# Kernel tuning notes

Hardware: AMD Instinct MI355X
Metric: run time of the kernel (lower is better)

Reference implementation:

```python
import jax, jax.numpy as jnp
import numpy as np


def _normalize(x):
    # channel mean-subtract then channel L2 normalize, as in MIDMs.forward
    x = x - x.mean(axis=1, keepdims=True)
    return x / jnp.linalg.norm(x, axis=1, keepdims=True)


def setup_inputs() -> dict:
    key = jax.random.key(0)
    ks = jax.random.split(key, 6)
    B, C, H, W = 2, 256, 64, 64
    return {
        "trg_out": jax.random.normal(ks[0], (B, C, H, W), jnp.float32),
        "src_out": jax.random.normal(ks[1], (B, C, H, W), jnp.float32),
        "ref_out": jax.random.normal(ks[2], (B, C, H, W), jnp.float32),
        "src_feats": jax.random.normal(ks[3], (B, 4, H, W), jnp.float32),
        "ref_feats": jax.random.normal(ks[4], (B, 4, H, W), jnp.float32),
        "ref_semantics": jax.random.uniform(ks[5], (B, 151, H, W), jnp.float32),
    }


def reference(trg_out, src_out, ref_out, src_feats, ref_feats, ref_semantics):
    B, C, H, W = trg_out.shape
    L = H * W
    # normalized matching features, flattened over spatial positions
    t = _normalize(trg_out).reshape(B, C, L)   # [B, C, Lt]
    s = _normalize(src_out).reshape(B, C, L)   # [B, C, Ls]
    r = _normalize(ref_out).reshape(B, C, L)

    # Correlation.correlation: dense cosine affinity between all position pairs
    corr_src = jnp.einsum("bci,bcj->bij", t, s)  # [B, Lt, Ls]
    corr_ref = jnp.einsum("bci,bcj->bij", t, r)

    # soft_warp: softmax over source positions, attention-weighted gather
    attn_src = jax.nn.softmax(corr_src, axis=-1)
    attn_ref = jax.nn.softmax(corr_ref, axis=-1)

    warped_src_feat = jnp.einsum("bij,bcj->bci", attn_src,
                                 src_feats.reshape(B, -1, L)).reshape(B, -1, H, W)
    warped_ref_feat = jnp.einsum("bij,bcj->bci", attn_ref,
                                 ref_feats.reshape(B, -1, L)).reshape(B, -1, H, W)
    warped_ref_seg = jnp.einsum("bij,bcj->bci", attn_ref,
                                ref_semantics.reshape(B, -1, L)).reshape(B, -1, H, W)
    return warped_src_feat, warped_ref_feat, warped_ref_seg
```

## Files before the change

### kernel.cpp

```cpp
#include <hip/hip_runtime.h>
#include <hip/hip_bf16.h>
#include <cstdint>
#include <cstddef>

typedef unsigned short u16;
typedef __attribute__((ext_vector_type(8))) __bf16 bf16x8;
typedef __attribute__((ext_vector_type(4))) unsigned u32x4;
typedef __attribute__((ext_vector_type(16))) float f32x16;

#define LPOS 4096
#define CDIM 256
#define LDSBUF 13312

#if __has_builtin(__builtin_amdgcn_exp2f)
#define EXP2(x) __builtin_amdgcn_exp2f(x)
#else
#define EXP2(x) exp2f(x)
#endif

#define GLOAD_LDS16(g, l)                                                      \
  __builtin_amdgcn_global_load_lds(                                            \
      (const __attribute__((address_space(1))) void*)(g),                      \
      (__attribute__((address_space(3))) void*)(l), 16, 0, 0)

__device__ __forceinline__ unsigned f2bfbits(float x) {
  union { float f; unsigned u; } v; v.f = x;
  return (v.u + 0x7FFFu + ((v.u >> 16) & 1u)) >> 16;
}
__device__ __forceinline__ unsigned packbf(float a, float b) {
  __hip_bfloat162 h2 = __float22bfloat162_rn(make_float2(a, b));
  return *(unsigned*)&h2;
}

__global__ void norm_fused(const float* __restrict__ t_in,
                           const float* __restrict__ s_in,
                           const float* __restrict__ r_in,
                           u16* __restrict__ qn, u16* __restrict__ ksn,
                           u16* __restrict__ krn) {
  __shared__ float tile[256 * 33];
  __shared__ float sums[256], sqs[256];
  __shared__ float mv[32], ivv[32];
  int idx = blockIdx.x;
  int ab = idx >> 7, lt = idx & 127;
  int arr = ab >> 1, b = ab & 1;
  int l0 = lt * 32;
  const float* inp = (arr == 0 ? t_in : arr == 1 ? s_in : r_in) + (size_t)b * CDIM * LPOS;
  u16* outp = (arr == 0 ? qn : arr == 1 ? ksn : krn) + (size_t)b * LPOS * CDIM;
  float scale = (arr == 0) ? 1.4426950408889634f : 1.0f;
  int t = threadIdx.x;
  int cg = t >> 5, l = t & 31;
  float sum = 0.f, sq = 0.f;
#pragma unroll 8
  for (int cc = 0; cc < 32; ++cc) {
    int c = cg * 32 + cc;
    float v = inp[(size_t)c * LPOS + l0 + l];
    tile[c * 33 + l] = v;
    sum += v; sq += v * v;
  }
  sums[t] = sum; sqs[t] = sq;
  __syncthreads();
  if (t < 32) {
    float s = 0.f, q = 0.f;
#pragma unroll
    for (int g = 0; g < 8; ++g) { s += sums[g * 32 + t]; q += sqs[g * 32 + t]; }
    float mean = s * (1.0f / CDIM);
    float nsq = q - s * s * (1.0f / CDIM);
    mv[t] = mean;
    ivv[t] = rsqrtf(fmaxf(nsq, 1e-20f)) * scale;
  }
  __syncthreads();
  int c2 = t & 127, ph = t >> 7;
#pragma unroll 4
  for (int rr = 0; rr < 16; ++rr) {
    int pos = ph + rr * 2;
    float m = mv[pos], iv = ivv[pos];
    float v0 = (tile[(2 * c2) * 33 + pos] - m) * iv;
    float v1 = (tile[(2 * c2 + 1) * 33 + pos] - m) * iv;
    *(unsigned*)&outp[(size_t)(l0 + pos) * CDIM + 2 * c2] = packbf(v0, v1);
  }
}

__global__ void build_v(const float* __restrict__ sf, const float* __restrict__ rf,
                        const float* __restrict__ sem,
                        u16* __restrict__ vs, u16* __restrict__ vr) {
  int t = blockIdx.x * 256 + threadIdx.x;
  const int NVS = 2 * 32 * 4096;
  if (t < NVS) {
    int b = t >> 17;
    int c = (t >> 12) & 31;
    int j = t & 4095;
    float v = (c < 4) ? sf[((size_t)b * 4 + c) * LPOS + j] : (c == 4 ? 1.0f : 0.0f);
    vs[t] = (u16)f2bfbits(v);
  } else {
    int t2 = t - NVS;
    if (t2 < 2 * 160 * 4096) {
      int b = t2 / (160 * 4096);
      int rr = t2 % (160 * 4096);
      int c = rr >> 12, j = rr & 4095;
      float v = (c < 151) ? sem[((size_t)b * 151 + c) * LPOS + j]
              : (c < 155) ? rf[((size_t)b * 4 + (c - 151)) * LPOS + j]
              : (c == 155) ? 1.0f : 0.0f;
      vr[((size_t)b * 160 + c) * LPOS + j] = (u16)f2bfbits(v);
    }
  }
}

template <int CT>
__device__ __forceinline__ void flash_body(
    const u16* __restrict__ qb, const u16* __restrict__ kb,
    const u16* __restrict__ vb, float* __restrict__ dst,
    u16 (*lds)[LDSBUF], int wave, int lane, int i_wave, int j_base, int iters) {
  int h = lane >> 5, ln = lane & 31;

  bf16x8 qf[16];
  const u16* qrow = qb + (size_t)(i_wave + ln) * CDIM;
#pragma unroll
  for (int kt = 0; kt < 16; ++kt)
    qf[kt] = *(const bf16x8*)(qrow + kt * 16 + h * 8);
#pragma unroll
  for (int kt = 0; kt < 16; ++kt)
    asm volatile("" : "+v"(*(u32x4*)&qf[kt]));

  f32x16 O[CT];
#pragma unroll
  for (int c = 0; c < CT; ++c)
#pragma unroll
    for (int t = 0; t < 16; ++t) O[c][t] = 0.0f;

  auto stage = [&](int j0s, int buf) {
#pragma unroll
    for (int g = 0; g < 4; ++g) {
      int G = wave * 4 + g;
      int j = 2 * G + h;
      GLOAD_LDS16(kb + (size_t)(j0s + j) * CDIM + (ln ^ (j & 7)) * 8,
                  &lds[buf][G * 512]);
    }
    if constexpr (CT == 5) {
#pragma unroll
      for (int g = 0; g < 3; ++g) {
        int s = wave + g * 4;
        if (s < 10) {
          int f = s * 64 + lane;
          int p = f / 160;
          int c = f - p * 160;
          GLOAD_LDS16(vb + (size_t)c * LPOS + j0s + p * 8,
                      &lds[buf][8192 + s * 512]);
        }
      }
    }
  };

  int kread_base = ln * 256 + 8 * (h ^ (ln & 1));
  int q = (ln >> 1) & 3;
  const u16* ka[4];
#pragma unroll
  for (int m = 0; m < 4; ++m) ka[m] = &lds[0][kread_base + 16 * (m ^ q)];
  const u16* va = &lds[0][8192 + h * 1280 + ln * 8];

  f32x16 Sp;
#pragma unroll
  for (int t = 0; t < 16; ++t) Sp[t] = 0.0f;

  auto finish_prev = [&](int pbo, const bf16x8* vfp) {
    f32x16 S;
#pragma unroll
    for (int t = 0; t < 16; ++t) S[t] = EXP2(Sp[t]);
    bf16x8 pb[2];
#pragma unroll
    for (int kh = 0; kh < 2; ++kh) {
      unsigned c0 = packbf(S[kh * 8 + 0], S[kh * 8 + 1]);
      unsigned c1 = packbf(S[kh * 8 + 2], S[kh * 8 + 3]);
      unsigned c2 = packbf(S[kh * 8 + 4], S[kh * 8 + 5]);
      unsigned c3 = packbf(S[kh * 8 + 6], S[kh * 8 + 7]);
      asm("v_permlane32_swap_b32 %0, %1" : "+v"(c0), "+v"(c2));
      asm("v_permlane32_swap_b32 %0, %1" : "+v"(c1), "+v"(c3));
      union { unsigned u[4]; bf16x8 v; } tmp;
      tmp.u[0] = c0;
      tmp.u[1] = c1;
      tmp.u[2] = c2;
      tmp.u[3] = c3;
      pb[kh] = tmp.v;
    }
#pragma unroll
    for (int ct = 0; ct < CT; ++ct)
#pragma unroll
      for (int kt2 = 0; kt2 < 2; ++kt2) {
        bf16x8 vax;
        if constexpr (CT == 5)
          vax = *(const bf16x8*)(va + kt2 * 2560 + ct * 256 + pbo);
        else
          vax = vfp[kt2];
        O[ct] = __builtin_amdgcn_mfma_f32_32x32x16_bf16(vax, pb[kt2], O[ct], 0, 0, 0);
      }
  };

  stage(j_base, 0);

  int buf = 0, pbo = 0;
  for (int jt = 0; jt < iters; ++jt) {
    int j0 = j_base + jt * 32;
    int bo = buf * LDSBUF;

    asm volatile("s_waitcnt vmcnt(0)" ::: "memory");
    __builtin_amdgcn_sched_barrier(0);
    __builtin_amdgcn_s_barrier();
    __builtin_amdgcn_sched_barrier(0);

    bf16x8 vf[2];
    if (CT == 1 && jt >= 1) {
#pragma unroll
      for (int kt2 = 0; kt2 < 2; ++kt2)
        vf[kt2] = *(const bf16x8*)(vb + (size_t)ln * LPOS + (j0 - 32) + (2 * kt2 + h) * 8);
    }
    if (jt + 1 < iters) {
      int nb = (buf == 2) ? 0 : buf + 1;
      stage(j0 + 32, nb);
    }

    __builtin_amdgcn_s_setprio(1);

    f32x16 Sa, Sb;
#pragma unroll
    for (int t = 0; t < 16; ++t) { Sa[t] = 0.0f; Sb[t] = 0.0f; }
#pragma unroll
    for (int kt = 0; kt < 16; kt += 2) {
      bf16x8 ka0 = *(const bf16x8*)(ka[kt & 3] + 64 * (kt >> 2) + bo);
      Sa = __builtin_amdgcn_mfma_f32_32x32x16_bf16(ka0, qf[kt], Sa, 0, 0, 0);
      bf16x8 ka1 = *(const bf16x8*)(ka[(kt + 1) & 3] + 64 * ((kt + 1) >> 2) + bo);
      Sb = __builtin_amdgcn_mfma_f32_32x32x16_bf16(ka1, qf[kt + 1], Sb, 0, 0, 0);
    }

    if (jt >= 1) finish_prev(pbo, vf);

#pragma unroll
    for (int t = 0; t < 16; ++t) Sp[t] = Sa[t] + Sb[t];

    __builtin_amdgcn_s_setprio(0);

    pbo = bo;
    buf = (buf == 2) ? 0 : buf + 1;
  }

  {
    bf16x8 vf[2];
    if constexpr (CT == 1) {
      int jlast = j_base + (iters - 1) * 32;
#pragma unroll
      for (int kt2 = 0; kt2 < 2; ++kt2)
        vf[kt2] = *(const bf16x8*)(vb + (size_t)ln * LPOS + jlast + (2 * kt2 + h) * 8);
    }
    finish_prev(pbo, vf);
  }

  const int climit = (CT == 1) ? 5 : 156;
#pragma unroll
  for (int ct = 0; ct < CT; ++ct)
#pragma unroll
    for (int t = 0; t < 16; ++t) {
      int c = ct * 32 + (t & 3) + 8 * (t >> 2) + 4 * h;
      if (c < climit)
        dst[(size_t)c * LPOS + i_wave + ln] = O[ct][t];
    }
}

__global__ __launch_bounds__(256, 2) void flash(
    const u16* __restrict__ qn, const u16* __restrict__ ksn, const u16* __restrict__ krn,
    const u16* __restrict__ vs, const u16* __restrict__ vr,
    float* __restrict__ nsrc, float* __restrict__ nref,
    int nch_src, int nch_ref) {
  __shared__ u16 lds[3][LDSBUF];
  int tid = threadIdx.x;
  int wave = tid >> 6, lane = tid & 63;
  int idx = blockIdx.x;
  int nrefb = 64 * nch_ref;
  if (idx < nrefb) {
    int r = idx;
    int chunk = r >> 6, b = (r >> 5) & 1, wgi = r & 31;
    int jchunk = LPOS / nch_ref;
    flash_body<5>(qn + (size_t)b * LPOS * CDIM, krn + (size_t)b * LPOS * CDIM,
                  vr + (size_t)b * 160 * LPOS,
                  nref + (size_t)(chunk * 2 + b) * 160 * LPOS,
                  lds, wave, lane, wgi * 128 + wave * 32, chunk * jchunk,
                  jchunk / 32);
  } else {
    int r = idx - nrefb;
    int chunk = r >> 6, b = (r >> 5) & 1, wgi = r & 31;
    int jchunk = LPOS / nch_src;
    flash_body<1>(qn + (size_t)b * LPOS * CDIM, ksn + (size_t)b * LPOS * CDIM,
                  vs + (size_t)b * 32 * LPOS,
                  nsrc + (size_t)(chunk * 2 + b) * 32 * LPOS,
                  lds, wave, lane, wgi * 128 + wave * 32, chunk * jchunk,
                  jchunk / 32);
  }
}

__global__ void finalize(const float* __restrict__ nsrc, const float* __restrict__ nref,
                         float* __restrict__ out, int nch_src, int nch_ref) {
  int v = blockIdx.x * 256 + threadIdx.x;
  if (v >= 325632) return;
  float nx = 0.f, ny = 0.f, nz = 0.f, nw = 0.f;
  float dx = 0.f, dy = 0.f, dz = 0.f, dw = 0.f;
  if (v < 8192) {
    int b = v >> 12, c = (v >> 10) & 3, i4 = v & 1023;
    for (int k = 0; k < nch_src; ++k) {
      const float* base = nsrc + ((size_t)(k * 2 + b) * 32) * LPOS;
      float4 n4 = ((const float4*)(base + (size_t)c * LPOS))[i4];
      float4 d4 = ((const float4*)(base + (size_t)4 * LPOS))[i4];
      nx += n4.x; ny += n4.y; nz += n4.z; nw += n4.w;
      dx += d4.x; dy += d4.y; dz += d4.z; dw += d4.w;
    }
  } else if (v < 16384) {
    int v1 = v - 8192;
    int b = v1 >> 12, c = (v1 >> 10) & 3, i4 = v1 & 1023;
    for (int k = 0; k < nch_ref; ++k) {
      const float* base = nref + ((size_t)(k * 2 + b) * 160) * LPOS;
      float4 n4 = ((const float4*)(base + (size_t)(151 + c) * LPOS))[i4];
      float4 d4 = ((const float4*)(base + (size_t)155 * LPOS))[i4];
      nx += n4.x; ny += n4.y; nz += n4.z; nw += n4.w;
      dx += d4.x; dy += d4.y; dz += d4.z; dw += d4.w;
    }
  } else {
    int v2 = v - 16384;
    int b = v2 / 154624;
    int rr = v2 - b * 154624;
    int c = rr >> 10, i4 = rr & 1023;
    for (int k = 0; k < nch_ref; ++k) {
      const float* base = nref + ((size_t)(k * 2 + b) * 160) * LPOS;
      float4 n4 = ((const float4*)(base + (size_t)c * LPOS))[i4];
      float4 d4 = ((const float4*)(base + (size_t)155 * LPOS))[i4];
      nx += n4.x; ny += n4.y; nz += n4.z; nw += n4.w;
      dx += d4.x; dy += d4.y; dz += d4.z; dw += d4.w;
    }
  }
  float4 r;
  r.x = nx / dx; r.y = ny / dy; r.z = nz / dz; r.w = nw / dw;
  ((float4*)out)[v] = r;
}

extern "C" void kernel_launch(void* const* d_in, const int* in_sizes, int n_in,
                              void* d_out, int out_size, void* d_ws, size_t ws_size,
                              hipStream_t stream) {
  const float* trg  = (const float*)d_in[0];
  const float* srcp = (const float*)d_in[1];
  const float* refp = (const float*)d_in[2];
  const float* sfeat = (const float*)d_in[3];
  const float* rfeat = (const float*)d_in[4];
  const float* rsem  = (const float*)d_in[5];
  float* out = (float*)d_out;

  char* ws = (char*)d_ws;
  size_t o = 0;
  auto alloc = [&](size_t bytes) -> char* {
    char* p = ws + o;
    o += (bytes + 255) & ~(size_t)255;
    return p;
  };
  u16* qn  = (u16*)alloc(2ull * LPOS * CDIM * 2);
  u16* ksn = (u16*)alloc(2ull * LPOS * CDIM * 2);
  u16* krn = (u16*)alloc(2ull * LPOS * CDIM * 2);
  u16* vs  = (u16*)alloc(2ull * 32 * LPOS * 2);
  u16* vr  = (u16*)alloc(2ull * 160 * LPOS * 2);

  size_t fixed = o;
  int nch_ref = 8;
  for (;;) {
    size_t need = fixed + 512 +
                  (size_t)nch_ref * 2 * 32 * LPOS * 4 +
                  (size_t)nch_ref * 2 * 160 * LPOS * 4;
    if (need <= ws_size || nch_ref == 1) break;
    nch_ref >>= 1;
  }
  int nch_src = nch_ref;
  float* nsrc = (float*)alloc((size_t)nch_src * 2 * 32 * LPOS * 4);
  float* nref = (float*)alloc((size_t)nch_ref * 2 * 160 * LPOS * 4);

  hipLaunchKernelGGL(norm_fused, dim3(768), dim3(256), 0, stream,
                     trg, srcp, refp, qn, ksn, krn);
  hipLaunchKernelGGL(build_v, dim3(6144), dim3(256), 0, stream,
                     sfeat, rfeat, rsem, vs, vr);
  hipLaunchKernelGGL(flash, dim3(64 * (nch_ref + nch_src)), dim3(256), 0, stream,
                     qn, ksn, krn, vs, vr, nsrc, nref, nch_src, nch_ref);
  hipLaunchKernelGGL(finalize, dim3(1272), dim3(256), 0, stream,
                     nsrc, nref, out, nch_src, nch_ref);
}
```

Measured before the change: 145.3 us.

## Split flash kernel into separate ref and src kernels with lighter src variant

The single fused flash kernel, which chose the ref or src path per block, becomes two launches. The src kernel double-buffers into smaller LDS with launch bounds for three blocks per CU, and the src key range is split into twice as many chunks. The aim is to stop the light src path from inheriting the ref path's large LDS and register footprint, which limited its occupancy. In exchange there is an extra kernel launch, the two paths can no longer overlap within one grid, and the finalize step has more src partials to reduce.

```diff
diff --git a/kernel.cpp b/kernel.cpp
--- a/kernel.cpp
+++ b/kernel.cpp
@@ -11,6 +11,7 @@
 #define LPOS 4096
 #define CDIM 256
 #define LDSBUF 13312
+#define LDSBUF_S 8192
 
 #if __has_builtin(__builtin_amdgcn_exp2f)
 #define EXP2(x) __builtin_amdgcn_exp2f(x)
@@ -105,12 +106,12 @@
   }
 }
 
-template <int CT>
-__device__ __forceinline__ void flash_body(
+__device__ __forceinline__ void flash_ref_body(
     const u16* __restrict__ qb, const u16* __restrict__ kb,
     const u16* __restrict__ vb, float* __restrict__ dst,
     u16 (*lds)[LDSBUF], int wave, int lane, int i_wave, int j_base, int iters) {
   int h = lane >> 5, ln = lane & 31;
+  const int CT = 5;
 
   bf16x8 qf[16];
   const u16* qrow = qb + (size_t)(i_wave + ln) * CDIM;
@@ -135,17 +136,15 @@
       GLOAD_LDS16(kb + (size_t)(j0s + j) * CDIM + (ln ^ (j & 7)) * 8,
                   &lds[buf][G * 512]);
     }
-    if constexpr (CT == 5) {
-#pragma unroll
-      for (int g = 0; g < 3; ++g) {
-        int s = wave + g * 4;
-        if (s < 10) {
-          int f = s * 64 + lane;
-          int p = f / 160;
-          int c = f - p * 160;
-          GLOAD_LDS16(vb + (size_t)c * LPOS + j0s + p * 8,
-                      &lds[buf][8192 + s * 512]);
-        }
+#pragma unroll
+    for (int g = 0; g < 3; ++g) {
+      int s = wave + g * 4;
+      if (s < 10) {
+        int f = s * 64 + lane;
+        int p = f / 160;
+        int c = f - p * 160;
+        GLOAD_LDS16(vb + (size_t)c * LPOS + j0s + p * 8,
+                    &lds[buf][8192 + s * 512]);
       }
     }
   };
@@ -161,7 +160,7 @@
 #pragma unroll
   for (int t = 0; t < 16; ++t) Sp[t] = 0.0f;
 
-  auto finish_prev = [&](int pbo, const bf16x8* vfp) {
+  auto finish_prev = [&](int pbo) {
     f32x16 S;
 #pragma unroll
     for (int t = 0; t < 16; ++t) S[t] = EXP2(Sp[t]);
@@ -175,21 +174,14 @@
       asm("v_permlane32_swap_b32 %0, %1" : "+v"(c0), "+v"(c2));
       asm("v_permlane32_swap_b32 %0, %1" : "+v"(c1), "+v"(c3));
       union { unsigned u[4]; bf16x8 v; } tmp;
-      tmp.u[0] = c0;
-      tmp.u[1] = c1;
-      tmp.u[2] = c2;
-      tmp.u[3] = c3;
+      tmp.u[0] = c0; tmp.u[1] = c1; tmp.u[2] = c2; tmp.u[3] = c3;
       pb[kh] = tmp.v;
     }
 #pragma unroll
     for (int ct = 0; ct < CT; ++ct)
 #pragma unroll
       for (int kt2 = 0; kt2 < 2; ++kt2) {
-        bf16x8 vax;
-        if constexpr (CT == 5)
-          vax = *(const bf16x8*)(va + kt2 * 2560 + ct * 256 + pbo);
-        else
-          vax = vfp[kt2];
+        bf16x8 vax = *(const bf16x8*)(va + kt2 * 2560 + ct * 256 + pbo);
         O[ct] = __builtin_amdgcn_mfma_f32_32x32x16_bf16(vax, pb[kt2], O[ct], 0, 0, 0);
       }
   };
@@ -206,12 +198,6 @@
     __builtin_amdgcn_s_barrier();
     __builtin_amdgcn_sched_barrier(0);
 
-    bf16x8 vf[2];
-    if (CT == 1 && jt >= 1) {
-#pragma unroll
-      for (int kt2 = 0; kt2 < 2; ++kt2)
-        vf[kt2] = *(const bf16x8*)(vb + (size_t)ln * LPOS + (j0 - 32) + (2 * kt2 + h) * 8);
-    }
     if (jt + 1 < iters) {
       int nb = (buf == 2) ? 0 : buf + 1;
       stage(j0 + 32, nb);
@@ -230,7 +216,7 @@
       Sb = __builtin_amdgcn_mfma_f32_32x32x16_bf16(ka1, qf[kt + 1], Sb, 0, 0, 0);
     }
 
-    if (jt >= 1) finish_prev(pbo, vf);
+    if (jt >= 1) finish_prev(pbo);
 
 #pragma unroll
     for (int t = 0; t < 16; ++t) Sp[t] = Sa[t] + Sb[t];
@@ -241,18 +227,9 @@
     buf = (buf == 2) ? 0 : buf + 1;
   }
 
-  {
-    bf16x8 vf[2];
-    if constexpr (CT == 1) {
-      int jlast = j_base + (iters - 1) * 32;
-#pragma unroll
-      for (int kt2 = 0; kt2 < 2; ++kt2)
-        vf[kt2] = *(const bf16x8*)(vb + (size_t)ln * LPOS + jlast + (2 * kt2 + h) * 8);
-    }
-    finish_prev(pbo, vf);
-  }
-
-  const int climit = (CT == 1) ? 5 : 156;
+  finish_prev(pbo);
+
+  const int climit = 156;
 #pragma unroll
   for (int ct = 0; ct < CT; ++ct)
 #pragma unroll
@@ -263,34 +240,152 @@
     }
 }
 
-__global__ __launch_bounds__(256, 2) void flash(
-    const u16* __restrict__ qn, const u16* __restrict__ ksn, const u16* __restrict__ krn,
-    const u16* __restrict__ vs, const u16* __restrict__ vr,
-    float* __restrict__ nsrc, float* __restrict__ nref,
-    int nch_src, int nch_ref) {
+__global__ __launch_bounds__(256, 2) void flash_ref(
+    const u16* __restrict__ qn, const u16* __restrict__ krn,
+    const u16* __restrict__ vr, float* __restrict__ nref, int nch_ref) {
   __shared__ u16 lds[3][LDSBUF];
   int tid = threadIdx.x;
   int wave = tid >> 6, lane = tid & 63;
-  int idx = blockIdx.x;
-  int nrefb = 64 * nch_ref;
-  if (idx < nrefb) {
-    int r = idx;
-    int chunk = r >> 6, b = (r >> 5) & 1, wgi = r & 31;
-    int jchunk = LPOS / nch_ref;
-    flash_body<5>(qn + (size_t)b * LPOS * CDIM, krn + (size_t)b * LPOS * CDIM,
-                  vr + (size_t)b * 160 * LPOS,
-                  nref + (size_t)(chunk * 2 + b) * 160 * LPOS,
-                  lds, wave, lane, wgi * 128 + wave * 32, chunk * jchunk,
-                  jchunk / 32);
-  } else {
-    int r = idx - nrefb;
-    int chunk = r >> 6, b = (r >> 5) & 1, wgi = r & 31;
-    int jchunk = LPOS / nch_src;
-    flash_body<1>(qn + (size_t)b * LPOS * CDIM, ksn + (size_t)b * LPOS * CDIM,
-                  vs + (size_t)b * 32 * LPOS,
-                  nsrc + (size_t)(chunk * 2 + b) * 32 * LPOS,
-                  lds, wave, lane, wgi * 128 + wave * 32, chunk * jchunk,
-                  jchunk / 32);
+  int r = blockIdx.x;
+  int chunk = r >> 6, b = (r >> 5) & 1, wgi = r & 31;
+  int jchunk = LPOS / nch_ref;
+  flash_ref_body(qn + (size_t)b * LPOS * CDIM, krn + (size_t)b * LPOS * CDIM,
+                 vr + (size_t)b * 160 * LPOS,
+                 nref + (size_t)(chunk * 2 + b) * 160 * LPOS,
+                 lds, wave, lane, wgi * 128 + wave * 32, chunk * jchunk,
+                 jchunk / 32);
+}
+
+__global__ __launch_bounds__(256, 3) void flash_src(
+    const u16* __restrict__ qn, const u16* __restrict__ ksn,
+    const u16* __restrict__ vs, float* __restrict__ nsrc, int nch_src) {
+  __shared__ u16 lds[2][LDSBUF_S];
+  int tid = threadIdx.x;
+  int wave = tid >> 6, lane = tid & 63;
+  int h = lane >> 5, ln = lane & 31;
+  int r = blockIdx.x;
+  int chunk = r >> 6, b = (r >> 5) & 1, wgi = r & 31;
+  int jchunk = LPOS / nch_src;
+  int iters = jchunk / 32;
+  int i_wave = wgi * 128 + wave * 32;
+  int j_base = chunk * jchunk;
+  const u16* qb = qn + (size_t)b * LPOS * CDIM;
+  const u16* kb = ksn + (size_t)b * LPOS * CDIM;
+  const u16* vb = vs + (size_t)b * 32 * LPOS;
+  float* dst = nsrc + (size_t)(chunk * 2 + b) * 32 * LPOS;
+
+  bf16x8 qf[16];
+  const u16* qrow = qb + (size_t)(i_wave + ln) * CDIM;
+#pragma unroll
+  for (int kt = 0; kt < 16; ++kt)
+    qf[kt] = *(const bf16x8*)(qrow + kt * 16 + h * 8);
+#pragma unroll
+  for (int kt = 0; kt < 16; ++kt)
+    asm volatile("" : "+v"(*(u32x4*)&qf[kt]));
+
+  f32x16 O;
+#pragma unroll
+  for (int t = 0; t < 16; ++t) O[t] = 0.0f;
+
+  auto stage = [&](int j0s, int buf) {
+#pragma unroll
+    for (int g = 0; g < 4; ++g) {
+      int G = wave * 4 + g;
+      int j = 2 * G + h;
+      GLOAD_LDS16(kb + (size_t)(j0s + j) * CDIM + (ln ^ (j & 7)) * 8,
+                  &lds[buf][G * 512]);
+    }
+  };
+
+  int kread_base = ln * 256 + 8 * (h ^ (ln & 1));
+  int q = (ln >> 1) & 3;
+  const u16* ka[4];
+#pragma unroll
+  for (int m = 0; m < 4; ++m) ka[m] = &lds[0][kread_base + 16 * (m ^ q)];
+
+  f32x16 Sp;
+#pragma unroll
+  for (int t = 0; t < 16; ++t) Sp[t] = 0.0f;
+
+  auto finish_prev = [&](const bf16x8* vfp) {
+    f32x16 S;
+#pragma unroll
+    for (int t = 0; t < 16; ++t) S[t] = EXP2(Sp[t]);
+    bf16x8 pb[2];
+#pragma unroll
+    for (int kh = 0; kh < 2; ++kh) {
+      unsigned c0 = packbf(S[kh * 8 + 0], S[kh * 8 + 1]);
+      unsigned c1 = packbf(S[kh * 8 + 2], S[kh * 8 + 3]);
+      unsigned c2 = packbf(S[kh * 8 + 4], S[kh * 8 + 5]);
+      unsigned c3 = packbf(S[kh * 8 + 6], S[kh * 8 + 7]);
+      asm("v_permlane32_swap_b32 %0, %1" : "+v"(c0), "+v"(c2));
+      asm("v_permlane32_swap_b32 %0, %1" : "+v"(c1), "+v"(c3));
+      union { unsigned u[4]; bf16x8 v; } tmp;
+      tmp.u[0] = c0; tmp.u[1] = c1; tmp.u[2] = c2; tmp.u[3] = c3;
+      pb[kh] = tmp.v;
+    }
+#pragma unroll
+    for (int kt2 = 0; kt2 < 2; ++kt2)
+      O = __builtin_amdgcn_mfma_f32_32x32x16_bf16(vfp[kt2], pb[kt2], O, 0, 0, 0);
+  };
+
+  stage(j_base, 0);
+
+  int buf = 0;
+  for (int jt = 0; jt < iters; ++jt) {
+    int j0 = j_base + jt * 32;
+    int bo = buf * LDSBUF_S;
+
+    asm volatile("s_waitcnt vmcnt(0)" ::: "memory");
+    __builtin_amdgcn_sched_barrier(0);
+    __builtin_amdgcn_s_barrier();
+    __builtin_amdgcn_sched_barrier(0);
+
+    bf16x8 vf[2];
+    if (jt >= 1) {
+#pragma unroll
+      for (int kt2 = 0; kt2 < 2; ++kt2)
+        vf[kt2] = *(const bf16x8*)(vb + (size_t)ln * LPOS + (j0 - 32) + (2 * kt2 + h) * 8);
+    }
+    if (jt + 1 < iters) stage(j0 + 32, buf ^ 1);
+
+    __builtin_amdgcn_s_setprio(1);
+
+    f32x16 Sa, Sb;
+#pragma unroll
+    for (int t = 0; t < 16; ++t) { Sa[t] = 0.0f; Sb[t] = 0.0f; }
+#pragma unroll
+    for (int kt = 0; kt < 16; kt += 2) {
+      bf16x8 ka0 = *(const bf16x8*)(ka[kt & 3] + 64 * (kt >> 2) + bo);
+      Sa = __builtin_amdgcn_mfma_f32_32x32x16_bf16(ka0, qf[kt], Sa, 0, 0, 0);
+      bf16x8 ka1 = *(const bf16x8*)(ka[(kt + 1) & 3] + 64 * ((kt + 1) >> 2) + bo);
+      Sb = __builtin_amdgcn_mfma_f32_32x32x16_bf16(ka1, qf[kt + 1], Sb, 0, 0, 0);
+    }
+
+    if (jt >= 1) finish_prev(vf);
+
+#pragma unroll
+    for (int t = 0; t < 16; ++t) Sp[t] = Sa[t] + Sb[t];
+
+    __builtin_amdgcn_s_setprio(0);
+
+    buf ^= 1;
+  }
+
+  {
+    bf16x8 vf[2];
+    int jlast = j_base + (iters - 1) * 32;
+#pragma unroll
+    for (int kt2 = 0; kt2 < 2; ++kt2)
+      vf[kt2] = *(const bf16x8*)(vb + (size_t)ln * LPOS + jlast + (2 * kt2 + h) * 8);
+    finish_prev(vf);
+  }
+
+#pragma unroll
+  for (int t = 0; t < 16; ++t) {
+    int c = (t & 3) + 8 * (t >> 2) + 4 * h;
+    if (c < 5)
+      dst[(size_t)c * LPOS + i_wave + ln] = O[t];
   }
 }
 
@@ -365,12 +460,12 @@
   int nch_ref = 8;
   for (;;) {
     size_t need = fixed + 512 +
-                  (size_t)nch_ref * 2 * 32 * LPOS * 4 +
+                  (size_t)(2 * nch_ref) * 2 * 32 * LPOS * 4 +
                   (size_t)nch_ref * 2 * 160 * LPOS * 4;
     if (need <= ws_size || nch_ref == 1) break;
     nch_ref >>= 1;
   }
-  int nch_src = nch_ref;
+  int nch_src = 2 * nch_ref;
   float* nsrc = (float*)alloc((size_t)nch_src * 2 * 32 * LPOS * 4);
   float* nref = (float*)alloc((size_t)nch_ref * 2 * 160 * LPOS * 4);
 
@@ -378,8 +473,10 @@
                      trg, srcp, refp, qn, ksn, krn);
   hipLaunchKernelGGL(build_v, dim3(6144), dim3(256), 0, stream,
                      sfeat, rfeat, rsem, vs, vr);
-  hipLaunchKernelGGL(flash, dim3(64 * (nch_ref + nch_src)), dim3(256), 0, stream,
-                     qn, ksn, krn, vs, vr, nsrc, nref, nch_src, nch_ref);
+  hipLaunchKernelGGL(flash_ref, dim3(64 * nch_ref), dim3(256), 0, stream,
+                     qn, krn, vr, nref, nch_ref);
+  hipLaunchKernelGGL(flash_src, dim3(64 * nch_src), dim3(256), 0, stream,
+                     qn, ksn, vs, nsrc, nch_src);
   hipLaunchKernelGGL(finalize, dim3(1272), dim3(256), 0, stream,
                      nsrc, nref, out, nch_src, nch_ref);
 }
```

Result: slower. 157.2 us (+8.2%).
